# Optimization experiments

Hardware: AMD Instinct MI355X
Metric: run time of the kernel (lower is better)

The kernel has to match this reference:

```python
import jax, jax.numpy as jnp
import numpy as np

JOINT_NUM = 25   # len(smpl_x.pos_joint_part['body'])
HM_D, HM_H, HM_W = 8, 8, 8
FEAT_DIM = 768


def setup_inputs() -> dict:
    key = jax.random.key(0)
    k1, k2, k3 = jax.random.split(key, 3)
    B = 512
    img_feat = jax.random.normal(k1, (B, FEAT_DIM, HM_H, HM_W), dtype=jnp.float32)
    out_ch = JOINT_NUM * HM_D  # 200
    # Conv2d 1x1 weight [out_ch, in_ch] and bias [out_ch]
    scale = 1.0 / np.sqrt(FEAT_DIM)
    conv_w = jax.random.uniform(k2, (out_ch, FEAT_DIM), jnp.float32, -scale, scale)
    conv_b = jax.random.uniform(k3, (out_ch,), jnp.float32, -scale, scale)
    return {"img_feat": img_feat, "conv_w": conv_w, "conv_b": conv_b}


def reference(img_feat, conv_w, conv_b):
    B = img_feat.shape[0]
    # 1x1 conv == per-pixel matmul over channels: bchw,oc -> bohw
    hm = jnp.einsum('bchw,oc->bohw', img_feat, conv_w) + conv_b[None, :, None, None]
    joint_hm_logits = hm.reshape(B, JOINT_NUM, HM_D, HM_H, HM_W)
    # softmax over flattened D*H*W
    flat = joint_hm_logits.reshape(B, JOINT_NUM, HM_D * HM_H * HM_W)
    p = jax.nn.softmax(flat, axis=2).reshape(B, JOINT_NUM, HM_D, HM_H, HM_W)
    # soft-argmax: marginal expectations along each axis
    accu_x = p.sum(axis=(2, 3))  # [B, J, W]
    accu_y = p.sum(axis=(2, 4))  # [B, J, H]
    accu_z = p.sum(axis=(3, 4))  # [B, J, D]
    x = (accu_x * jnp.arange(HM_W, dtype=jnp.float32)).sum(axis=2, keepdims=True)
    y = (accu_y * jnp.arange(HM_H, dtype=jnp.float32)).sum(axis=2, keepdims=True)
    z = (accu_z * jnp.arange(HM_D, dtype=jnp.float32)).sum(axis=2, keepdims=True)
    joint_coord = jnp.concatenate((x, y, z), axis=2)  # [B, J, 3]
    # original recomputes the same softmax for the returned heatmap
    joint_hm = p
    return (joint_hm, joint_coord)
```

## Files before the change

kernel.cpp:

```cpp
#include <hip/hip_runtime.h>


typedef __attribute__((ext_vector_type(4))) float f32x4;
typedef __attribute__((ext_vector_type(8))) short bf16x8;
typedef __attribute__((ext_vector_type(4))) unsigned int u32x4;

namespace {
constexpr int kB = 512, kC = 768, kP = 64, kO = 200, kJ = 25;
constexpr int kKT = 32, kSteps = 24;
constexpr int kNP = 224, kNT = 13;
constexpr int kAR = 40;
constexpr int kHR = 67;
constexpr int kWsHalf = kSteps * kNP * kKT;
constexpr size_t kHmOut = (size_t)kB * kJ * 512;
constexpr int kOffAlo = kP * kAR * 2;
constexpr int kSmemBytes = kO * kHR * 4;
}

__device__ inline unsigned short f2bf(float x) {
  union { float f; unsigned u; } c; c.f = x;
  unsigned r = c.u + 0x7FFFu + ((c.u >> 16) & 1u);
  return (unsigned short)(r >> 16);
}
__device__ inline float bf2f(unsigned short h) {
  union { unsigned u; float f; } c; c.u = ((unsigned)h) << 16;
  return c.f;
}

__global__ __launch_bounds__(256) void weight_split_kernel(
    const float* __restrict__ w, unsigned short* __restrict__ ws) {
  const int id = blockIdx.x * 256 + threadIdx.x;
  if (id >= kSteps * kNP * 8) return;
  const int t = id / (kNP * 8);
  const int rem = id - t * (kNP * 8);
  const int n = rem >> 3;
  const int kk = (rem & 7) * 4;
  f32x4 v = {0.f, 0.f, 0.f, 0.f};
  if (n < kO) v = *(const f32x4*)(w + (size_t)n * kC + t * kKT + kk);
  unsigned short hi[4], lo[4];
#pragma unroll
  for (int i = 0; i < 4; ++i) {
    hi[i] = f2bf(v[i]);
    lo[i] = f2bf(v[i] - bf2f(hi[i]));
  }
  const size_t base = (size_t)(t * kNP + n) * kKT + kk;
  typedef __attribute__((ext_vector_type(4))) unsigned short us4;
  *(us4*)(ws + base) = us4{hi[0], hi[1], hi[2], hi[3]};
  *(us4*)(ws + kWsHalf + base) = us4{lo[0], lo[1], lo[2], lo[3]};
}

__global__ __launch_bounds__(256, 2) void posnet_fused_kernel(
    const float* __restrict__ img, const unsigned short* __restrict__ wsb,
    const float* __restrict__ bias, float* __restrict__ out) {
  __shared__ __align__(16) char smem[kSmemBytes];
  __shared__ float ldsBias[kO];
  unsigned short* ldsAhi = (unsigned short*)smem;
  unsigned short* ldsAlo = (unsigned short*)(smem + kOffAlo);
  float* hm = (float*)smem;

  const int b = blockIdx.x;
  const int tid = threadIdx.x;
  const int lane = tid & 63;
  const int wid = tid >> 6;
  const float* __restrict__ imgb = img + (size_t)b * kC * kP;

  if (tid < kO) ldsBias[tid] = bias[tid];

  const int m_l = lane & 15;
  const int g = lane >> 4;
  const int kk0 = g * 8;

  f32x4 acc[4][4];
#pragma unroll
  for (int i = 0; i < 4; ++i)
#pragma unroll
    for (int j = 0; j < 4; ++j) acc[i][j] = f32x4{0.f, 0.f, 0.f, 0.f};

  const int sp = tid & 63;
  const int sc0 = (tid >> 6) * 8;

  for (int t = 0; t < kSteps; ++t) {
    __syncthreads();
    {
      const float* src = imgb + (size_t)(t * kKT + sc0) * kP + sp;
      unsigned u[8];
#pragma unroll
      for (int i = 0; i < 8; ++i) u[i] = __float_as_uint(src[(size_t)i * kP]);
      unsigned ph[4], pl[4];
#pragma unroll
      for (int i = 0; i < 4; ++i) {
        const unsigned a = u[2 * i], c = u[2 * i + 1];
        const unsigned am = a & 0xFFFF0000u, cm = c & 0xFFFF0000u;
        ph[i] = (a >> 16) | cm;
        const float la = __uint_as_float(a) - __uint_as_float(am);
        const float lc = __uint_as_float(c) - __uint_as_float(cm);
        pl[i] = (__float_as_uint(la) >> 16) | (__float_as_uint(lc) & 0xFFFF0000u);
      }
      *(u32x4*)(ldsAhi + sp * kAR + sc0) = u32x4{ph[0], ph[1], ph[2], ph[3]};
      *(u32x4*)(ldsAlo + sp * kAR + sc0) = u32x4{pl[0], pl[1], pl[2], pl[3]};
    }
    bf16x8 bhi[4], blo[4];
#pragma unroll
    for (int ni = 0; ni < 4; ++ni) {
      const int nt = ni * 4 + wid;
      if (nt < kNT) {
        const unsigned short* bs =
            wsb + ((size_t)t * kNP + nt * 16 + m_l) * kKT + kk0;
        bhi[ni] = *(const bf16x8*)bs;
        blo[ni] = *(const bf16x8*)(bs + kWsHalf);
      }
    }
    __syncthreads();
    bf16x8 ahi[4], alo[4];
#pragma unroll
    for (int mt = 0; mt < 4; ++mt) {
      const int row = mt * 16 + m_l;
      ahi[mt] = *(const bf16x8*)(ldsAhi + row * kAR + kk0);
      alo[mt] = *(const bf16x8*)(ldsAlo + row * kAR + kk0);
    }
#pragma unroll
    for (int ni = 0; ni < 4; ++ni) {
      const int nt = ni * 4 + wid;
      if (nt < kNT) {
#pragma unroll
        for (int mt = 0; mt < 4; ++mt) {
          acc[ni][mt] = __builtin_amdgcn_mfma_f32_16x16x32_bf16(
              ahi[mt], bhi[ni], acc[ni][mt], 0, 0, 0);
          acc[ni][mt] = __builtin_amdgcn_mfma_f32_16x16x32_bf16(
              ahi[mt], blo[ni], acc[ni][mt], 0, 0, 0);
          acc[ni][mt] = __builtin_amdgcn_mfma_f32_16x16x32_bf16(
              alo[mt], bhi[ni], acc[ni][mt], 0, 0, 0);
        }
      }
    }
  }
  __syncthreads();

#pragma unroll
  for (int ni = 0; ni < 4; ++ni) {
    const int nt = ni * 4 + wid;
    if (nt < kNT) {
      const int o = nt * 16 + m_l;
      if (o < kO) {
        const float bo = ldsBias[o];
#pragma unroll
        for (int mt = 0; mt < 4; ++mt) {
          const int m = mt * 16 + g * 4;
#pragma unroll
          for (int r = 0; r < 4; ++r) hm[o * kHR + m + r] = acc[ni][mt][r] + bo;
        }
      }
    }
  }
  __syncthreads();

  for (int j = wid; j < kJ; j += 4) {
    float v[8];
#pragma unroll
    for (int k = 0; k < 8; ++k) v[k] = hm[(j * 8 + k) * kHR + lane];

    float m = v[0];
#pragma unroll
    for (int k = 1; k < 8; ++k) m = fmaxf(m, v[k]);
#pragma unroll
    for (int off = 32; off > 0; off >>= 1) m = fmaxf(m, __shfl_xor(m, off));

    float e[8];
    float s = 0.f;
#pragma unroll
    for (int k = 0; k < 8; ++k) {
      e[k] = __expf(v[k] - m);
      s += e[k];
    }
#pragma unroll
    for (int off = 32; off > 0; off >>= 1) s += __shfl_xor(s, off);
    const float inv = 1.0f / s;

    float psum = 0.f, zsum = 0.f;
    float* dst = out + ((size_t)b * kJ + j) * 512;
#pragma unroll
    for (int k = 0; k < 8; ++k) {
      const float pv = e[k] * inv;
      dst[k * 64 + lane] = pv;
      psum += pv;
      zsum += (float)k * pv;
    }
    float xs = (float)(lane & 7) * psum;
    float ys = (float)(lane >> 3) * psum;
#pragma unroll
    for (int off = 32; off > 0; off >>= 1) {
      xs += __shfl_xor(xs, off);
      ys += __shfl_xor(ys, off);
      zsum += __shfl_xor(zsum, off);
    }
    if (lane == 0) {
      float* cd = out + kHmOut + ((size_t)b * kJ + j) * 3;
      cd[0] = xs;
      cd[1] = ys;
      cd[2] = zsum;
    }
  }
}

extern "C" void kernel_launch(void* const* d_in, const int* in_sizes, int n_in,
                              void* d_out, int out_size, void* d_ws,
                              size_t ws_size, hipStream_t stream) {
  const float* img = (const float*)d_in[0];
  const float* w = (const float*)d_in[1];
  const float* bias = (const float*)d_in[2];
  unsigned short* wsb = (unsigned short*)d_ws;
  float* out = (float*)d_out;

  const int pre_tasks = kSteps * kNP * 8;
  weight_split_kernel<<<dim3((pre_tasks + 255) / 256), dim3(256), 0, stream>>>(w, wsb);
  posnet_fused_kernel<<<dim3(kB), dim3(256), 0, stream>>>(img, wsb, bias, out);
}
```

Baseline: 177.9 us.

## Split fused kernel into pipelined GEMM and separate softmax pass

Reworks the GEMM with a K tile of 64, double-buffered LDS holding the img hi/lo split, and register prefetch of the next tile so global loads overlap the MFMAs. The weights are pre-packed directly into MFMA fragment order, so each B load becomes one contiguous per-lane vector. The GEMM now writes raw logits to the output buffer and a separate kernel does the in-place softmax and soft-argmax, which lowers LDS use so three blocks can run per CU. The cost is an extra global round trip of the heatmap plus an extra kernel launch.

After: 199.4 us. 12.1% more time.

```diff
diff --git a/kernel.cpp b/kernel.cpp
--- a/kernel.cpp
+++ b/kernel.cpp
@@ -3,18 +3,15 @@
 
 typedef __attribute__((ext_vector_type(4))) float f32x4;
 typedef __attribute__((ext_vector_type(8))) short bf16x8;
+typedef __attribute__((ext_vector_type(4))) unsigned short us4;
 typedef __attribute__((ext_vector_type(4))) unsigned int u32x4;
 
 namespace {
 constexpr int kB = 512, kC = 768, kP = 64, kO = 200, kJ = 25;
-constexpr int kKT = 32, kSteps = 24;
-constexpr int kNP = 224, kNT = 13;
-constexpr int kAR = 40;
-constexpr int kHR = 67;
-constexpr int kWsHalf = kSteps * kNP * kKT;
+constexpr int kKT = 64, kSteps = 12;
+constexpr int kNT = 13, kNTP = 14;
+constexpr int kWsHalf = 12 * 2 * 14 * 512;
 constexpr size_t kHmOut = (size_t)kB * kJ * 512;
-constexpr int kOffAlo = kP * kAR * 2;
-constexpr int kSmemBytes = kO * kHR * 4;
 }
 
 __device__ inline unsigned short f2bf(float x) {
@@ -30,45 +27,55 @@
 __global__ __launch_bounds__(256) void weight_split_kernel(
     const float* __restrict__ w, unsigned short* __restrict__ ws) {
   const int id = blockIdx.x * 256 + threadIdx.x;
-  if (id >= kSteps * kNP * 8) return;
-  const int t = id / (kNP * 8);
-  const int rem = id - t * (kNP * 8);
-  const int n = rem >> 3;
-  const int kk = (rem & 7) * 4;
-  f32x4 v = {0.f, 0.f, 0.f, 0.f};
-  if (n < kO) v = *(const f32x4*)(w + (size_t)n * kC + t * kKT + kk);
-  unsigned short hi[4], lo[4];
-#pragma unroll
-  for (int i = 0; i < 4; ++i) {
-    hi[i] = f2bf(v[i]);
-    lo[i] = f2bf(v[i] - bf2f(hi[i]));
-  }
-  const size_t base = (size_t)(t * kNP + n) * kKT + kk;
-  typedef __attribute__((ext_vector_type(4))) unsigned short us4;
-  *(us4*)(ws + base) = us4{hi[0], hi[1], hi[2], hi[3]};
-  *(us4*)(ws + kWsHalf + base) = us4{lo[0], lo[1], lo[2], lo[3]};
-}
-
-__global__ __launch_bounds__(256, 2) void posnet_fused_kernel(
+  if (id >= 43008) return;
+  const int ml = id & 15, g = (id >> 4) & 3;
+  const int id2 = id >> 6;
+  const int nt = id2 % 14;
+  const int q = id2 / 14;
+  const int kc = q & 1;
+  const int q2 = q >> 1;
+  const int t = q2 % 12;
+  const int half = q2 / 12;
+  const int n = nt * 16 + ml;
+  const int kb = t * 64 + kc * 32 + g * 8;
+  float v[8];
+#pragma unroll
+  for (int i = 0; i < 8; ++i)
+    v[i] = (n < kO) ? w[(size_t)n * kC + kb + i] : 0.f;
+  unsigned short o8[8];
+#pragma unroll
+  for (int i = 0; i < 8; ++i) {
+    const unsigned short hi = f2bf(v[i]);
+    o8[i] = half ? f2bf(v[i] - bf2f(hi)) : hi;
+  }
+  unsigned short* dst =
+      ws + (size_t)half * kWsHalf +
+      ((((size_t)(t * 2 + kc) * 14 + nt) * 4 + g) * 16 + ml) * 8;
+  *(us4*)dst = us4{o8[0], o8[1], o8[2], o8[3]};
+  *(us4*)(dst + 4) = us4{o8[4], o8[5], o8[6], o8[7]};
+}
+
+__device__ inline int afrag(int buf, int half, int kc, int g, int px) {
+  return ((((buf * 2 + half) * 2 + kc) * 4 + g) * 64 + px) * 16;
+}
+
+__global__ __launch_bounds__(256, 3) void gemm_kernel(
     const float* __restrict__ img, const unsigned short* __restrict__ wsb,
     const float* __restrict__ bias, float* __restrict__ out) {
-  __shared__ __align__(16) char smem[kSmemBytes];
-  __shared__ float ldsBias[kO];
-  unsigned short* ldsAhi = (unsigned short*)smem;
-  unsigned short* ldsAlo = (unsigned short*)(smem + kOffAlo);
-  float* hm = (float*)smem;
+  __shared__ __align__(16) char smem[32768];
 
   const int b = blockIdx.x;
   const int tid = threadIdx.x;
   const int lane = tid & 63;
   const int wid = tid >> 6;
-  const float* __restrict__ imgb = img + (size_t)b * kC * kP;
-
-  if (tid < kO) ldsBias[tid] = bias[tid];
-
   const int m_l = lane & 15;
   const int g = lane >> 4;
-  const int kk0 = g * 8;
+  const float* __restrict__ imgb = img + (size_t)b * kC * kP;
+
+  const int px = lane;
+  const int c0 = wid * 16;
+  const int skc = c0 >> 5;
+  const int sg0 = (c0 & 31) >> 3;
 
   f32x4 acc[4][4];
 #pragma unroll
@@ -76,65 +83,71 @@
 #pragma unroll
     for (int j = 0; j < 4; ++j) acc[i][j] = f32x4{0.f, 0.f, 0.f, 0.f};
 
-  const int sp = tid & 63;
-  const int sc0 = (tid >> 6) * 8;
+  float pf[16];
+
+  auto load_pf = [&](int t) {
+#pragma unroll
+    for (int i = 0; i < 16; ++i)
+      pf[i] = imgb[(size_t)(t * kKT + c0 + i) * kP + px];
+  };
+  auto split_write = [&](int buf) {
+    unsigned ph[8], pl[8];
+#pragma unroll
+    for (int i = 0; i < 8; ++i) {
+      const unsigned a = __float_as_uint(pf[2 * i]);
+      const unsigned c = __float_as_uint(pf[2 * i + 1]);
+      const unsigned am = a & 0xFFFF0000u, cm = c & 0xFFFF0000u;
+      ph[i] = (a >> 16) | cm;
+      const float la = __uint_as_float(a) - __uint_as_float(am);
+      const float lc = __uint_as_float(c) - __uint_as_float(cm);
+      pl[i] = (__float_as_uint(la) >> 16) | (__float_as_uint(lc) & 0xFFFF0000u);
+    }
+    *(u32x4*)(smem + afrag(buf, 0, skc, sg0, px)) = u32x4{ph[0], ph[1], ph[2], ph[3]};
+    *(u32x4*)(smem + afrag(buf, 0, skc, sg0 + 1, px)) = u32x4{ph[4], ph[5], ph[6], ph[7]};
+    *(u32x4*)(smem + afrag(buf, 1, skc, sg0, px)) = u32x4{pl[0], pl[1], pl[2], pl[3]};
+    *(u32x4*)(smem + afrag(buf, 1, skc, sg0 + 1, px)) = u32x4{pl[4], pl[5], pl[6], pl[7]};
+  };
+
+  load_pf(0);
+  split_write(0);
+  __syncthreads();
 
   for (int t = 0; t < kSteps; ++t) {
-    __syncthreads();
-    {
-      const float* src = imgb + (size_t)(t * kKT + sc0) * kP + sp;
-      unsigned u[8];
-#pragma unroll
-      for (int i = 0; i < 8; ++i) u[i] = __float_as_uint(src[(size_t)i * kP]);
-      unsigned ph[4], pl[4];
-#pragma unroll
-      for (int i = 0; i < 4; ++i) {
-        const unsigned a = u[2 * i], c = u[2 * i + 1];
-        const unsigned am = a & 0xFFFF0000u, cm = c & 0xFFFF0000u;
-        ph[i] = (a >> 16) | cm;
-        const float la = __uint_as_float(a) - __uint_as_float(am);
-        const float lc = __uint_as_float(c) - __uint_as_float(cm);
-        pl[i] = (__float_as_uint(la) >> 16) | (__float_as_uint(lc) & 0xFFFF0000u);
+    const int buf = t & 1;
+    if (t + 1 < kSteps) load_pf(t + 1);
+
+#pragma unroll
+    for (int kc = 0; kc < 2; ++kc) {
+      bf16x8 ah[4], al[4];
+#pragma unroll
+      for (int mt = 0; mt < 4; ++mt) {
+        ah[mt] = *(const bf16x8*)(smem + afrag(buf, 0, kc, g, mt * 16 + m_l));
+        al[mt] = *(const bf16x8*)(smem + afrag(buf, 1, kc, g, mt * 16 + m_l));
       }
-      *(u32x4*)(ldsAhi + sp * kAR + sc0) = u32x4{ph[0], ph[1], ph[2], ph[3]};
-      *(u32x4*)(ldsAlo + sp * kAR + sc0) = u32x4{pl[0], pl[1], pl[2], pl[3]};
-    }
-    bf16x8 bhi[4], blo[4];
-#pragma unroll
-    for (int ni = 0; ni < 4; ++ni) {
-      const int nt = ni * 4 + wid;
-      if (nt < kNT) {
-        const unsigned short* bs =
-            wsb + ((size_t)t * kNP + nt * 16 + m_l) * kKT + kk0;
-        bhi[ni] = *(const bf16x8*)bs;
-        blo[ni] = *(const bf16x8*)(bs + kWsHalf);
+#pragma unroll
+      for (int ni = 0; ni < 4; ++ni) {
+        const int nt = ni * 4 + wid;
+        if (nt < kNT) {
+          const unsigned short* bp =
+              wsb + ((size_t)(t * 2 + kc) * 14 + nt) * 512 + lane * 8;
+          const bf16x8 bh = *(const bf16x8*)bp;
+          const bf16x8 bl = *(const bf16x8*)(bp + kWsHalf);
+#pragma unroll
+          for (int mt = 0; mt < 4; ++mt) {
+            acc[ni][mt] = __builtin_amdgcn_mfma_f32_16x16x32_bf16(
+                ah[mt], bh, acc[ni][mt], 0, 0, 0);
+            acc[ni][mt] = __builtin_amdgcn_mfma_f32_16x16x32_bf16(
+                ah[mt], bl, acc[ni][mt], 0, 0, 0);
+            acc[ni][mt] = __builtin_amdgcn_mfma_f32_16x16x32_bf16(
+                al[mt], bh, acc[ni][mt], 0, 0, 0);
+          }
+        }
       }
     }
     __syncthreads();
-    bf16x8 ahi[4], alo[4];
-#pragma unroll
-    for (int mt = 0; mt < 4; ++mt) {
-      const int row = mt * 16 + m_l;
-      ahi[mt] = *(const bf16x8*)(ldsAhi + row * kAR + kk0);
-      alo[mt] = *(const bf16x8*)(ldsAlo + row * kAR + kk0);
-    }
-#pragma unroll
-    for (int ni = 0; ni < 4; ++ni) {
-      const int nt = ni * 4 + wid;
-      if (nt < kNT) {
-#pragma unroll
-        for (int mt = 0; mt < 4; ++mt) {
-          acc[ni][mt] = __builtin_amdgcn_mfma_f32_16x16x32_bf16(
-              ahi[mt], bhi[ni], acc[ni][mt], 0, 0, 0);
-          acc[ni][mt] = __builtin_amdgcn_mfma_f32_16x16x32_bf16(
-              ahi[mt], blo[ni], acc[ni][mt], 0, 0, 0);
-          acc[ni][mt] = __builtin_amdgcn_mfma_f32_16x16x32_bf16(
-              alo[mt], bhi[ni], acc[ni][mt], 0, 0, 0);
-        }
-      }
-    }
-  }
-  __syncthreads();
+    if (t + 1 < kSteps) split_write(buf ^ 1);
+    __syncthreads();
+  }
 
 #pragma unroll
   for (int ni = 0; ni < 4; ++ni) {
@@ -142,63 +155,68 @@
     if (nt < kNT) {
       const int o = nt * 16 + m_l;
       if (o < kO) {
-        const float bo = ldsBias[o];
+        const float bo = bias[o];
 #pragma unroll
         for (int mt = 0; mt < 4; ++mt) {
-          const int m = mt * 16 + g * 4;
-#pragma unroll
-          for (int r = 0; r < 4; ++r) hm[o * kHR + m + r] = acc[ni][mt][r] + bo;
+          f32x4 v;
+#pragma unroll
+          for (int r = 0; r < 4; ++r) v[r] = acc[ni][mt][r] + bo;
+          *(f32x4*)(out + ((size_t)b * kO + o) * 64 + mt * 16 + g * 4) = v;
         }
       }
     }
   }
-  __syncthreads();
-
-  for (int j = wid; j < kJ; j += 4) {
-    float v[8];
-#pragma unroll
-    for (int k = 0; k < 8; ++k) v[k] = hm[(j * 8 + k) * kHR + lane];
-
-    float m = v[0];
-#pragma unroll
-    for (int k = 1; k < 8; ++k) m = fmaxf(m, v[k]);
-#pragma unroll
-    for (int off = 32; off > 0; off >>= 1) m = fmaxf(m, __shfl_xor(m, off));
-
-    float e[8];
-    float s = 0.f;
-#pragma unroll
-    for (int k = 0; k < 8; ++k) {
-      e[k] = __expf(v[k] - m);
-      s += e[k];
-    }
-#pragma unroll
-    for (int off = 32; off > 0; off >>= 1) s += __shfl_xor(s, off);
-    const float inv = 1.0f / s;
-
-    float psum = 0.f, zsum = 0.f;
-    float* dst = out + ((size_t)b * kJ + j) * 512;
-#pragma unroll
-    for (int k = 0; k < 8; ++k) {
-      const float pv = e[k] * inv;
-      dst[k * 64 + lane] = pv;
-      psum += pv;
-      zsum += (float)k * pv;
-    }
-    float xs = (float)(lane & 7) * psum;
-    float ys = (float)(lane >> 3) * psum;
-#pragma unroll
-    for (int off = 32; off > 0; off >>= 1) {
-      xs += __shfl_xor(xs, off);
-      ys += __shfl_xor(ys, off);
-      zsum += __shfl_xor(zsum, off);
-    }
-    if (lane == 0) {
-      float* cd = out + kHmOut + ((size_t)b * kJ + j) * 3;
-      cd[0] = xs;
-      cd[1] = ys;
-      cd[2] = zsum;
-    }
+}
+
+__global__ __launch_bounds__(256) void softmax_kernel(float* __restrict__ out) {
+  const int b = blockIdx.x;
+  const int j = blockIdx.y * 4 + (threadIdx.x >> 6);
+  const int lane = threadIdx.x & 63;
+  if (j >= kJ) return;
+
+  float* base = out + ((size_t)b * kJ + j) * 512;
+  float v[8];
+#pragma unroll
+  for (int k = 0; k < 8; ++k) v[k] = base[k * 64 + lane];
+
+  float m = v[0];
+#pragma unroll
+  for (int k = 1; k < 8; ++k) m = fmaxf(m, v[k]);
+#pragma unroll
+  for (int off = 32; off > 0; off >>= 1) m = fmaxf(m, __shfl_xor(m, off));
+
+  float e[8];
+  float s = 0.f;
+#pragma unroll
+  for (int k = 0; k < 8; ++k) {
+    e[k] = __expf(v[k] - m);
+    s += e[k];
+  }
+#pragma unroll
+  for (int off = 32; off > 0; off >>= 1) s += __shfl_xor(s, off);
+  const float inv = 1.0f / s;
+
+  float psum = 0.f, zsum = 0.f;
+#pragma unroll
+  for (int k = 0; k < 8; ++k) {
+    const float pv = e[k] * inv;
+    base[k * 64 + lane] = pv;
+    psum += pv;
+    zsum += (float)k * pv;
+  }
+  float xs = (float)(lane & 7) * psum;
+  float ys = (float)(lane >> 3) * psum;
+#pragma unroll
+  for (int off = 32; off > 0; off >>= 1) {
+    xs += __shfl_xor(xs, off);
+    ys += __shfl_xor(ys, off);
+    zsum += __shfl_xor(zsum, off);
+  }
+  if (lane == 0) {
+    float* cd = out + kHmOut + ((size_t)b * kJ + j) * 3;
+    cd[0] = xs;
+    cd[1] = ys;
+    cd[2] = zsum;
   }
 }
 
@@ -211,7 +229,7 @@
   unsigned short* wsb = (unsigned short*)d_ws;
   float* out = (float*)d_out;
 
-  const int pre_tasks = kSteps * kNP * 8;
-  weight_split_kernel<<<dim3((pre_tasks + 255) / 256), dim3(256), 0, stream>>>(w, wsb);
-  posnet_fused_kernel<<<dim3(kB), dim3(256), 0, stream>>>(img, wsb, bias, out);
-}
+  weight_split_kernel<<<dim3(168), dim3(256), 0, stream>>>(w, wsb);
+  gemm_kernel<<<dim3(kB), dim3(256), 0, stream>>>(img, wsb, bias, out);
+  softmax_kernel<<<dim3(kB, 7), dim3(256), 0, stream>>>(out);
+}
```
